# Performance work log

Hardware: AMD Instinct MI355X
Metric: run time of the kernel (lower is better)

Reference implementation:

```python
import jax, jax.numpy as jnp
import numpy as np

EPS = 1e-5
TCOUNT = 18  # SBNet tiles per spatial dim -> 10x10 px tiles on 180x180 map
NUM_HEADS = 6
NUM_ATTRS = 5


def _conv(x, w, groups=1):
    # 3x3 stride-1 'SAME' conv, NCHW / OIHW
    return jax.lax.conv_general_dilated(
        x, w, window_strides=(1, 1), padding='SAME',
        dimension_numbers=('NCHW', 'OIHW', 'NCHW'),
        feature_group_count=groups)


def _bn(y, g, b, m, v):
    scale = g / jnp.sqrt(v + EPS)
    return y * scale[None, :, None, None] + (b - m * scale)[None, :, None, None]


def _mask_px(tile_mask, H, W):
    # expand [B, ty, tx] tile activity to per-pixel mask [B, 1, H, W]
    ty, tx = tile_mask.shape[1], tile_mask.shape[2]
    m = tile_mask.astype(jnp.float32)
    m = jnp.repeat(jnp.repeat(m, H // ty, axis=1), W // tx, axis=2)
    return m[:, None]


def setup_inputs() -> dict:
    key = jax.random.key(0)
    ks = jax.random.split(key, 24)
    B, C, H, W = 2, 512, 180, 180
    SC = 64                       # SHARED_CONV_CHANNEL
    HM1 = SC * NUM_HEADS          # 384
    HM2 = 2 * NUM_HEADS           # hm_max_ch * num_heads = 12
    AT1 = SC * NUM_HEADS * NUM_ATTRS  # 1920
    AT2 = 3 * NUM_ATTRS * NUM_HEADS   # attr_max_ch * 5 * 6 = 90

    def w(k, o, i):
        return jax.random.normal(k, (o, i, 3, 3), jnp.float32) * (1.0 / np.sqrt(i * 9))

    inp = {
        'x': jax.random.normal(ks[0], (B, C, H, W), jnp.float32),
        'tile_mask': jax.random.randint(ks[1], (B, TCOUNT, TCOUNT), 0, 2, jnp.int32),
        'w_shared': w(ks[2], SC, C),
        'g_s': jax.random.uniform(ks[3], (SC,), jnp.float32, 0.5, 1.5),
        'b_s': jax.random.normal(ks[4], (SC,)) * 0.1,
        'm_s': jax.random.normal(ks[5], (SC,)) * 0.1,
        'v_s': jax.random.uniform(ks[6], (SC,), jnp.float32, 0.5, 1.5),
        'w_hm1': w(ks[7], HM1, SC),
        'g_h': jax.random.uniform(ks[8], (HM1,), jnp.float32, 0.5, 1.5),
        'b_h': jax.random.normal(ks[9], (HM1,)) * 0.1,
        'm_h': jax.random.normal(ks[10], (HM1,)) * 0.1,
        'v_h': jax.random.uniform(ks[11], (HM1,), jnp.float32, 0.5, 1.5),
        'w_hm2': w(ks[12], HM2, SC),  # groups=6 -> in_per_group = 384/6 = 64
        'bias_hm': jnp.full((HM2,), -2.19, jnp.float32),  # fill_bias(-2.19)
        'w_attr1': w(ks[13], AT1, SC),
        'g_a': jax.random.uniform(ks[14], (AT1,), jnp.float32, 0.5, 1.5),
        'b_a': jax.random.normal(ks[15], (AT1,)) * 0.1,
        'm_a': jax.random.normal(ks[16], (AT1,)) * 0.1,
        'v_a': jax.random.uniform(ks[17], (AT1,), jnp.float32, 0.5, 1.5),
        'w_attr2': w(ks[18], AT2, SC),  # groups=30 -> in_per_group = 1920/30 = 64
        'bias_attr': jnp.zeros((AT2,), jnp.float32),
    }
    return inp


def reference(x, tile_mask, w_shared, g_s, b_s, m_s, v_s,
              w_hm1, g_h, b_h, m_h, v_h, w_hm2, bias_hm,
              w_attr1, g_a, b_a, m_a, v_a, w_attr2, bias_attr):
    B, _, H, W = x.shape
    mp = _mask_px(tile_mask, H, W)  # SBNet active-tile scatter mask

    # shared conv: gather active tiles -> conv -> BN -> ReLU -> scatter
    xg = x * mp
    shared = jax.nn.relu(_bn(_conv(xg, w_shared), g_s, b_s, m_s, v_s)) * mp

    # heatmap branch: Conv-BN-ReLU (64 -> 384, groups=1) then grouped conv (groups=6)
    h = jax.nn.relu(_bn(_conv(shared, w_hm1), g_h, b_h, m_h, v_h)) * mp
    hm = (_conv(h, w_hm2, groups=NUM_HEADS) + bias_hm[None, :, None, None]) * mp

    # attribute branch: Conv-BN-ReLU (64 -> 1920, groups=1) then grouped conv (groups=30)
    a = jax.nn.relu(_bn(_conv(shared, w_attr1), g_a, b_a, m_a, v_a)) * mp
    attr = (_conv(a, w_attr2, groups=NUM_HEADS * NUM_ATTRS)
            + bias_attr[None, :, None, None]) * mp

    # per-head slices are static index ranges of these tensors (heatmap_outp_inds /
    # attr_outp_inds); return the full stacked maps concatenated on channels.
    return jnp.concatenate([hm, attr], axis=1)  # [B, 12+90, H, W]
```

## Files before the change

kernel.cpp:

```cpp
#include <hip/hip_runtime.h>
#include <cstdint>

#define TC 18
#define HW 180
#define EPSF 1e-5f

typedef _Float16 half8 __attribute__((ext_vector_type(8)));
typedef _Float16 half4 __attribute__((ext_vector_type(4)));
typedef float f32x4 __attribute__((ext_vector_type(4)));

#define OFF_SHB  0
#define N_SHB    (2*HW*HW*64)
#define OFF_WSH  (N_SHB)
#define N_WSH    (9*64*512)
#define OFF_WM   (OFF_WSH + N_WSH)
#define N_WM     (36*9*64*64)
#define OFF_W2   (OFF_WM + N_WM)
#define N_W2     (36*9*16*64)

__global__ __launch_bounds__(256) void prep_kernel(
    const float* __restrict__ w_s, const float* __restrict__ w_hm1,
    const float* __restrict__ w_attr1, const float* __restrict__ w_hm2,
    const float* __restrict__ w_attr2, _Float16* __restrict__ ws) {
  int i = blockIdx.x * 256 + threadIdx.x;
  if (i < N_WSH) {
    int ic = i & 511, oc = (i >> 9) & 63, tap = i >> 15;
    ws[OFF_WSH + i] = (_Float16)w_s[((size_t)(oc*512 + ic))*9 + tap];
    return;
  }
  i -= N_WSH;
  if (i < N_WM) {
    int ic = i & 63, oc = (i >> 6) & 63, tap = (i >> 12) % 9, g = i / 36864;
    float v;
    if (g < 6) v = w_hm1[((size_t)((g*64 + oc)*64 + ic))*9 + tap];
    else       v = w_attr1[((size_t)(((g-6)*64 + oc)*64 + ic))*9 + tap];
    ws[OFF_WM + i] = (_Float16)v;
    return;
  }
  i -= N_WM;
  if (i < N_W2) {
    int ic = i & 63, oc = (i >> 6) & 15, tap = (i >> 10) % 9, g = i / 9216;
    float v = 0.f;
    if (g < 6) { if (oc < 2) v = w_hm2[((size_t)((g*2 + oc)*64 + ic))*9 + tap]; }
    else       { if (oc < 3) v = w_attr2[((size_t)(((g-6)*3 + oc)*64 + ic))*9 + tap]; }
    ws[OFF_W2 + i] = (_Float16)v;
  }
}

__global__ __launch_bounds__(256, 4) void shared_conv_mfma(
    const float* __restrict__ x, const int* __restrict__ tmask,
    const _Float16* __restrict__ wsh,
    const float* __restrict__ g_s, const float* __restrict__ b_s,
    const float* __restrict__ m_s, const float* __restrict__ v_s,
    _Float16* __restrict__ shb) {
  int bid = blockIdx.x;
  int b = bid / (TC*TC), t = bid % (TC*TC);
  int ty = t / TC, tx = t % TC;
  int Y0 = ty*10, X0 = tx*10;
  int tid = threadIdx.x;
  _Float16* shp = shb + (size_t)b*HW*HW*64;
  bool active = tmask[b*TC*TC + t] != 0;
  if (!active) {
    for (int i = tid; i < 1600; i += 256) {
      int px = i >> 4, q = i & 15;
      int gy = Y0 + px/10, gx = X0 + px%10;
      *(float2*)(shp + ((size_t)(gy*HW + gx))*64 + q*4) = make_float2(0.f, 0.f);
    }
    return;
  }
  int nact = 0;
  #pragma unroll
  for (int dy = 0; dy < 3; dy++)
    #pragma unroll
    for (int dx = 0; dx < 3; dx++) {
      int tyy = ty+dy-1, txx = tx+dx-1;
      int a = (tyy>=0 && tyy<TC && txx>=0 && txx<TC) ? tmask[b*TC*TC + tyy*TC + txx] : 0;
      nact |= (a != 0) << (dy*3+dx);
    }
  __shared__ _Float16 sm[144*64];
  int lane = tid & 63, w = tid >> 6;
  int mh = w >> 1, nh = w & 1;
  int l15 = lane & 15, l4 = lane >> 4;
  int r0[4];
  #pragma unroll
  for (int fi = 0; fi < 4; fi++) {
    int f = mh + fi*2;
    int p = f*16 + l15; if (p > 99) p = 99;
    r0[fi] = (p/10)*12 + (p%10);
  }
  f32x4 acc[4][2];
  #pragma unroll
  for (int fi = 0; fi < 4; fi++)
    #pragma unroll
    for (int j = 0; j < 2; j++) acc[fi][j] = (f32x4)0.f;

  for (int ck = 0; ck < 8; ck++) {
    __syncthreads();
    for (int i = tid; i < 1152; i += 256) {
      int px = i % 144, s8 = i / 144;
      int ry = px/12, rx = px%12;
      int gy = Y0-1+ry, gx = X0-1+rx;
      int selr = (ry==0)?0:((ry<=10)?1:2);
      int selc = (rx==0)?0:((rx<=10)?1:2);
      bool ok = (gy>=0 && gy<HW && gx>=0 && gx<HW) && ((nact>>(selr*3+selc))&1);
      half8 hv;
      #pragma unroll
      for (int j = 0; j < 8; j++) hv[j] = (_Float16)0.f;
      if (ok) {
        const float* xp = x + (((size_t)b*512 + ck*64 + s8*8)*HW + gy)*HW + gx;
        #pragma unroll
        for (int j = 0; j < 8; j++) hv[j] = (_Float16)xp[(size_t)j*HW*HW];
      }
      *(half8*)((char*)sm + px*128 + (((s8 ^ (px&7)) & 7)<<4)) = hv;
    }
    __syncthreads();
    for (int tap = 0; tap < 9; tap++) {
      int ky = tap/3, kx = tap%3;
      int radd = ky*12 + kx;
      #pragma unroll
      for (int ks = 0; ks < 2; ks++) {
        half8 bf[2];
        #pragma unroll
        for (int j = 0; j < 2; j++) {
          int oc = (nh*2 + j)*16 + l15;
          bf[j] = *(const half8*)(wsh + (size_t)(tap*64 + oc)*512 + ck*64 + ks*32 + l4*8);
        }
        #pragma unroll
        for (int fi = 0; fi < 4; fi++) {
          int f = mh + fi*2;
          if (f < 7) {
            int r = r0[fi] + radd;
            half8 af = *(const half8*)((const char*)sm + (r<<7) + ((((ks*4 + l4) ^ r) & 7)<<4));
            acc[fi][0] = __builtin_amdgcn_mfma_f32_16x16x32_f16(bf[0], af, acc[fi][0], 0, 0, 0);
            acc[fi][1] = __builtin_amdgcn_mfma_f32_16x16x32_f16(bf[1], af, acc[fi][1], 0, 0, 0);
          }
        }
      }
    }
  }
  float sc4[2][4], sh4[2][4];
  #pragma unroll
  for (int j = 0; j < 2; j++) {
    int ocb = (nh*2 + j)*16 + l4*4;
    float4 gg = *(const float4*)&g_s[ocb];
    float4 vv = *(const float4*)&v_s[ocb];
    float4 bb = *(const float4*)&b_s[ocb];
    float4 mm = *(const float4*)&m_s[ocb];
    float gA[4] = {gg.x,gg.y,gg.z,gg.w}, vA[4] = {vv.x,vv.y,vv.z,vv.w};
    float bA[4] = {bb.x,bb.y,bb.z,bb.w}, mA[4] = {mm.x,mm.y,mm.z,mm.w};
    #pragma unroll
    for (int r = 0; r < 4; r++) {
      float s = gA[r] * rsqrtf(vA[r] + EPSF);
      sc4[j][r] = s; sh4[j][r] = bA[r] - mA[r]*s;
    }
  }
  #pragma unroll
  for (int fi = 0; fi < 4; fi++) {
    int f = mh + fi*2;
    if (f < 7) {
      int p = f*16 + l15;
      if (p < 100) {
        int gy = Y0 + p/10, gx = X0 + p%10;
        _Float16* dst = shp + ((size_t)(gy*HW + gx))*64;
        #pragma unroll
        for (int j = 0; j < 2; j++) {
          int ocb = (nh*2 + j)*16 + l4*4;
          half4 hv;
          #pragma unroll
          for (int r = 0; r < 4; r++)
            hv[r] = (_Float16)fmaxf(fmaf(acc[fi][j][r], sc4[j][r], sh4[j][r]), 0.f);
          *(half4*)(dst + ocb) = hv;
        }
      }
    }
  }
}

__global__ __launch_bounds__(256, 3) void branch_conv_mfma(
    const _Float16* __restrict__ shb, const int* __restrict__ tmask,
    const _Float16* __restrict__ wm, const _Float16* __restrict__ w2,
    const float* __restrict__ g_h, const float* __restrict__ b_h,
    const float* __restrict__ m_h, const float* __restrict__ v_h,
    const float* __restrict__ g_a, const float* __restrict__ b_a,
    const float* __restrict__ m_a, const float* __restrict__ v_a,
    const float* __restrict__ bias_hm, const float* __restrict__ bias_attr,
    float* __restrict__ out) {
  int bid = blockIdx.x;
  int g = bid % 36;
  int t = bid / 36;
  int b = t / (TC*TC); t %= (TC*TC);
  int ty = t / TC, tx = t % TC;
  int Y0 = ty*10, X0 = tx*10;
  int tid = threadIdx.x;
  int Oc = (g < 6) ? 2 : 3;
  int cobase = (g < 6) ? g*2 : 12 + (g-6)*3;
  bool active = tmask[b*TC*TC + ty*TC + tx] != 0;
  if (!active) {
    if (tid < 100) {
      int py = tid/10, px = tid%10;
      for (int o = 0; o < Oc; o++)
        out[(((size_t)b*102 + cobase + o)*HW + (Y0+py))*HW + (X0+px)] = 0.f;
    }
    return;
  }
  int nact = 0;
  #pragma unroll
  for (int dy = 0; dy < 3; dy++)
    #pragma unroll
    for (int dx = 0; dx < 3; dx++) {
      int tyy = ty+dy-1, txx = tx+dx-1;
      int a = (tyy>=0 && tyy<TC && txx>=0 && txx<TC) ? tmask[b*TC*TC + tyy*TC + txx] : 0;
      nact |= (a != 0) << (dy*3+dx);
    }
  __shared__ _Float16 sm[196*64];
  const _Float16* shp = shb + (size_t)b*HW*HW*64;
  int lane = tid & 63, w = tid >> 6;
  int mh = w >> 1, nh = w & 1;
  int l15 = lane & 15, l4 = lane >> 4;

  for (int i = tid; i < 1568; i += 256) {
    int px = i >> 3, s8 = i & 7;
    int ry = px/14, rx = px%14;
    int gy = Y0-2+ry, gx = X0-2+rx;
    half8 hv;
    if (gy>=0 && gy<HW && gx>=0 && gx<HW)
      hv = *(const half8*)(shp + ((size_t)(gy*HW + gx))*64 + s8*8);
    else {
      #pragma unroll
      for (int j = 0; j < 8; j++) hv[j] = (_Float16)0.f;
    }
    *(half8*)((char*)sm + px*128 + (((s8 ^ px) & 7)<<4)) = hv;
  }
  __syncthreads();

  int r0[5];
  #pragma unroll
  for (int fi = 0; fi < 5; fi++) {
    int f = mh + fi*2;
    int p = f*16 + l15; if (p > 143) p = 143;
    r0[fi] = (p/12)*14 + (p%12);
  }
  f32x4 acc[5][2];
  #pragma unroll
  for (int fi = 0; fi < 5; fi++)
    #pragma unroll
    for (int j = 0; j < 2; j++) acc[fi][j] = (f32x4)0.f;

  const _Float16* wmg = wm + (size_t)g*9*64*64;
  for (int tap = 0; tap < 9; tap++) {
    int radd = (tap/3)*14 + (tap%3);
    #pragma unroll
    for (int ks = 0; ks < 2; ks++) {
      half8 bf[2];
      #pragma unroll
      for (int j = 0; j < 2; j++) {
        int oc = (nh*2 + j)*16 + l15;
        bf[j] = *(const half8*)(wmg + (size_t)(tap*64 + oc)*64 + ks*32 + l4*8);
      }
      #pragma unroll
      for (int fi = 0; fi < 5; fi++) {
        int f = mh + fi*2;
        if (f < 9) {
          int r = r0[fi] + radd;
          half8 af = *(const half8*)((const char*)sm + (r<<7) + ((((ks*4 + l4) ^ r) & 7)<<4));
          acc[fi][0] = __builtin_amdgcn_mfma_f32_16x16x32_f16(bf[0], af, acc[fi][0], 0, 0, 0);
          acc[fi][1] = __builtin_amdgcn_mfma_f32_16x16x32_f16(bf[1], af, acc[fi][1], 0, 0, 0);
        }
      }
    }
  }
  __syncthreads();

  {
    float sc4[2][4], sh4[2][4];
    #pragma unroll
    for (int j = 0; j < 2; j++) {
      int ocb = (nh*2 + j)*16 + l4*4;
      int c = ((g < 6) ? g*64 : (g-6)*64) + ocb;
      const float* Gp = (g < 6) ? g_h : g_a;
      const float* Vp = (g < 6) ? v_h : v_a;
      const float* Bp = (g < 6) ? b_h : b_a;
      const float* Mp = (g < 6) ? m_h : m_a;
      float4 gg = *(const float4*)&Gp[c];
      float4 vv = *(const float4*)&Vp[c];
      float4 bb = *(const float4*)&Bp[c];
      float4 mm = *(const float4*)&Mp[c];
      float gA[4] = {gg.x,gg.y,gg.z,gg.w}, vA[4] = {vv.x,vv.y,vv.z,vv.w};
      float bA[4] = {bb.x,bb.y,bb.z,bb.w}, mA[4] = {mm.x,mm.y,mm.z,mm.w};
      #pragma unroll
      for (int r = 0; r < 4; r++) {
        float s = gA[r] * rsqrtf(vA[r] + EPSF);
        sc4[j][r] = s; sh4[j][r] = bA[r] - mA[r]*s;
      }
    }
    #pragma unroll
    for (int fi = 0; fi < 5; fi++) {
      int f = mh + fi*2;
      if (f < 9) {
        int px = f*16 + l15;
        int hy = px/12, hx = px - hy*12;
        int selr = (hy==0)?0:((hy<=10)?1:2);
        int selc = (hx==0)?0:((hx<=10)?1:2);
        bool ok = (nact>>(selr*3+selc)) & 1;
        #pragma unroll
        for (int j = 0; j < 2; j++) {
          int ocb = (nh*2 + j)*16 + l4*4;
          half4 hv;
          #pragma unroll
          for (int r = 0; r < 4; r++) {
            float v = ok ? fmaxf(fmaf(acc[fi][j][r], sc4[j][r], sh4[j][r]), 0.f) : 0.f;
            hv[r] = (_Float16)v;
          }
          *(half4*)((char*)sm + (px<<7) + ((((ocb>>3) ^ px) & 7)<<4) + (ocb&7)*2) = hv;
        }
      }
    }
  }
  __syncthreads();

  int r0b[2];
  #pragma unroll
  for (int fi = 0; fi < 2; fi++) {
    int f = w + fi*4;
    int p = f*16 + l15; if (p > 99) p = 99;
    r0b[fi] = (p/10)*12 + (p%10);
  }
  f32x4 acc2[2];
  acc2[0] = (f32x4)0.f; acc2[1] = (f32x4)0.f;
  const _Float16* w2g = w2 + (size_t)g*9*16*64;
  for (int tap = 0; tap < 9; tap++) {
    int radd = (tap/3)*12 + (tap%3);
    #pragma unroll
    for (int ks = 0; ks < 2; ks++) {
      half8 bf = *(const half8*)(w2g + (size_t)(tap*16 + l15)*64 + ks*32 + l4*8);
      #pragma unroll
      for (int fi = 0; fi < 2; fi++) {
        int f = w + fi*4;
        if (f < 7) {
          int r = r0b[fi] + radd;
          half8 af = *(const half8*)((const char*)sm + (r<<7) + ((((ks*4 + l4) ^ r) & 7)<<4));
          acc2[fi] = __builtin_amdgcn_mfma_f32_16x16x32_f16(bf, af, acc2[fi], 0, 0, 0);
        }
      }
    }
  }
  float bo[3];
  #pragma unroll
  for (int o = 0; o < 3; o++)
    bo[o] = (o < Oc) ? ((g < 6) ? bias_hm[g*2 + o] : bias_attr[(g-6)*3 + o]) : 0.f;
  #pragma unroll
  for (int fi = 0; fi < 2; fi++) {
    int f = w + fi*4;
    int p = f*16 + l15;
    if (f < 7 && l4 == 0 && p < 100) {
      int gy = Y0 + p/10, gx = X0 + p%10;
      float* op = out + (((size_t)b*102 + cobase)*HW + gy)*HW + gx;
      #pragma unroll
      for (int o = 0; o < 3; o++)
        if (o < Oc) op[(size_t)o*HW*HW] = acc2[fi][o] + bo[o];
    }
  }
}

extern "C" void kernel_launch(void* const* d_in, const int* in_sizes, int n_in,
                              void* d_out, int out_size, void* d_ws, size_t ws_size,
                              hipStream_t stream) {
  const float* x        = (const float*)d_in[0];
  const int*   tmask    = (const int*)  d_in[1];
  const float* w_s      = (const float*)d_in[2];
  const float* g_s      = (const float*)d_in[3];
  const float* b_s      = (const float*)d_in[4];
  const float* m_s      = (const float*)d_in[5];
  const float* v_s      = (const float*)d_in[6];
  const float* w_hm1    = (const float*)d_in[7];
  const float* g_h      = (const float*)d_in[8];
  const float* b_h      = (const float*)d_in[9];
  const float* m_h      = (const float*)d_in[10];
  const float* v_h      = (const float*)d_in[11];
  const float* w_hm2    = (const float*)d_in[12];
  const float* bias_hm  = (const float*)d_in[13];
  const float* w_attr1  = (const float*)d_in[14];
  const float* g_a      = (const float*)d_in[15];
  const float* b_a      = (const float*)d_in[16];
  const float* m_a      = (const float*)d_in[17];
  const float* v_a      = (const float*)d_in[18];
  const float* w_attr2  = (const float*)d_in[19];
  const float* bias_attr= (const float*)d_in[20];
  _Float16* ws = (_Float16*)d_ws;
  float* out = (float*)d_out;

  int prep_total = N_WSH + N_WM + N_W2;
  prep_kernel<<<(prep_total + 255)/256, 256, 0, stream>>>(
      w_s, w_hm1, w_attr1, w_hm2, w_attr2, ws);
  shared_conv_mfma<<<2*TC*TC, 256, 0, stream>>>(
      x, tmask, ws + OFF_WSH, g_s, b_s, m_s, v_s, ws + OFF_SHB);
  branch_conv_mfma<<<2*TC*TC*36, 256, 0, stream>>>(
      ws + OFF_SHB, tmask, ws + OFF_WM, ws + OFF_W2,
      g_h, b_h, m_h, v_h, g_a, b_a, m_a, v_a, bias_hm, bias_attr, out);
}
```

Baseline: 658.6 us.

## Process two channel groups per block sharing one staged input halo tile

Each block of the branch conv now handles two of the 36 channel groups instead of one, so the shared-conv halo tile is loaded into LDS once for both groups and the grid is halved. Each wave pair computes all 64 output channels for one group, and the intermediate activations are written to two LDS buffers in two synchronized phases so that the second group does not overwrite the input still being read by the first. This removes half of the global-to-LDS staging traffic and the per-block setup cost. In exchange it uses more LDS and doubles the accumulator registers per wave (20 instead of 10 MFMA tiles), which may reduce occupancy under launch_bounds(256,3).

```diff
diff --git a/kernel.cpp b/kernel.cpp
--- a/kernel.cpp
+++ b/kernel.cpp
@@ -186,20 +186,24 @@
     const float* __restrict__ bias_hm, const float* __restrict__ bias_attr,
     float* __restrict__ out) {
   int bid = blockIdx.x;
-  int g = bid % 36;
-  int t = bid / 36;
+  int g2 = bid % 18;
+  int t = bid / 18;
   int b = t / (TC*TC); t %= (TC*TC);
   int ty = t / TC, tx = t % TC;
   int Y0 = ty*10, X0 = tx*10;
   int tid = threadIdx.x;
-  int Oc = (g < 6) ? 2 : 3;
-  int cobase = (g < 6) ? g*2 : 12 + (g-6)*3;
   bool active = tmask[b*TC*TC + ty*TC + tx] != 0;
   if (!active) {
     if (tid < 100) {
-      int py = tid/10, px = tid%10;
-      for (int o = 0; o < Oc; o++)
-        out[(((size_t)b*102 + cobase + o)*HW + (Y0+py))*HW + (X0+px)] = 0.f;
+      int py = tid/10, pxx = tid%10;
+      #pragma unroll
+      for (int gi = 0; gi < 2; gi++) {
+        int g = g2*2 + gi;
+        int Oc = (g < 6) ? 2 : 3;
+        int cobase = (g < 6) ? g*2 : 12 + (g-6)*3;
+        for (int o = 0; o < Oc; o++)
+          out[(((size_t)b*102 + cobase + o)*HW + (Y0+py))*HW + (X0+pxx)] = 0.f;
+      }
     }
     return;
   }
@@ -212,10 +216,11 @@
       int a = (tyy>=0 && tyy<TC && txx>=0 && txx<TC) ? tmask[b*TC*TC + tyy*TC + txx] : 0;
       nact |= (a != 0) << (dy*3+dx);
     }
-  __shared__ _Float16 sm[196*64];
+  __shared__ _Float16 sm[(196 + 144)*64];
   const _Float16* shp = shb + (size_t)b*HW*HW*64;
   int lane = tid & 63, w = tid >> 6;
-  int mh = w >> 1, nh = w & 1;
+  int gi = w & 1, m = w >> 1;
+  int g = g2*2 + gi;
   int l15 = lane & 15, l4 = lane >> 4;
 
   for (int i = tid; i < 1568; i += 256) {
@@ -236,97 +241,103 @@
   int r0[5];
   #pragma unroll
   for (int fi = 0; fi < 5; fi++) {
-    int f = mh + fi*2;
-    int p = f*16 + l15; if (p > 143) p = 143;
+    int gf = m*5 + fi;
+    int p = gf*16 + l15; if (p > 143) p = 143;
     r0[fi] = (p/12)*14 + (p%12);
   }
-  f32x4 acc[5][2];
+  f32x4 acc[5][4];
   #pragma unroll
   for (int fi = 0; fi < 5; fi++)
     #pragma unroll
-    for (int j = 0; j < 2; j++) acc[fi][j] = (f32x4)0.f;
+    for (int nf = 0; nf < 4; nf++) acc[fi][nf] = (f32x4)0.f;
 
   const _Float16* wmg = wm + (size_t)g*9*64*64;
   for (int tap = 0; tap < 9; tap++) {
     int radd = (tap/3)*14 + (tap%3);
     #pragma unroll
     for (int ks = 0; ks < 2; ks++) {
-      half8 bf[2];
-      #pragma unroll
-      for (int j = 0; j < 2; j++) {
-        int oc = (nh*2 + j)*16 + l15;
-        bf[j] = *(const half8*)(wmg + (size_t)(tap*64 + oc)*64 + ks*32 + l4*8);
-      }
+      half8 bf[4];
+      #pragma unroll
+      for (int nf = 0; nf < 4; nf++)
+        bf[nf] = *(const half8*)(wmg + (size_t)(tap*64 + nf*16 + l15)*64 + ks*32 + l4*8);
       #pragma unroll
       for (int fi = 0; fi < 5; fi++) {
-        int f = mh + fi*2;
-        if (f < 9) {
+        int gf = m*5 + fi;
+        if (gf < 9) {
           int r = r0[fi] + radd;
           half8 af = *(const half8*)((const char*)sm + (r<<7) + ((((ks*4 + l4) ^ r) & 7)<<4));
-          acc[fi][0] = __builtin_amdgcn_mfma_f32_16x16x32_f16(bf[0], af, acc[fi][0], 0, 0, 0);
-          acc[fi][1] = __builtin_amdgcn_mfma_f32_16x16x32_f16(bf[1], af, acc[fi][1], 0, 0, 0);
-        }
-      }
-    }
-  }
-  __syncthreads();
+          #pragma unroll
+          for (int nf = 0; nf < 4; nf++)
+            acc[fi][nf] = __builtin_amdgcn_mfma_f32_16x16x32_f16(bf[nf], af, acc[fi][nf], 0, 0, 0);
+        }
+      }
+    }
+  }
 
   {
-    float sc4[2][4], sh4[2][4];
-    #pragma unroll
-    for (int j = 0; j < 2; j++) {
-      int ocb = (nh*2 + j)*16 + l4*4;
-      int c = ((g < 6) ? g*64 : (g-6)*64) + ocb;
-      const float* Gp = (g < 6) ? g_h : g_a;
-      const float* Vp = (g < 6) ? v_h : v_a;
-      const float* Bp = (g < 6) ? b_h : b_a;
-      const float* Mp = (g < 6) ? m_h : m_a;
-      float4 gg = *(const float4*)&Gp[c];
-      float4 vv = *(const float4*)&Vp[c];
-      float4 bb = *(const float4*)&Bp[c];
-      float4 mm = *(const float4*)&Mp[c];
+    int cbase = (g < 6) ? g*64 : (g-6)*64;
+    const float* GG = (g < 6) ? g_h : g_a;
+    const float* VV = (g < 6) ? v_h : v_a;
+    const float* BB = (g < 6) ? b_h : b_a;
+    const float* MM = (g < 6) ? m_h : m_a;
+    float sc4[4][4], sh4[4][4];
+    #pragma unroll
+    for (int nf = 0; nf < 4; nf++) {
+      int c = cbase + nf*16 + l4*4;
+      float4 gg = *(const float4*)&GG[c];
+      float4 vv = *(const float4*)&VV[c];
+      float4 bb = *(const float4*)&BB[c];
+      float4 mm = *(const float4*)&MM[c];
       float gA[4] = {gg.x,gg.y,gg.z,gg.w}, vA[4] = {vv.x,vv.y,vv.z,vv.w};
       float bA[4] = {bb.x,bb.y,bb.z,bb.w}, mA[4] = {mm.x,mm.y,mm.z,mm.w};
       #pragma unroll
       for (int r = 0; r < 4; r++) {
         float s = gA[r] * rsqrtf(vA[r] + EPSF);
-        sc4[j][r] = s; sh4[j][r] = bA[r] - mA[r]*s;
-      }
-    }
-    #pragma unroll
-    for (int fi = 0; fi < 5; fi++) {
-      int f = mh + fi*2;
-      if (f < 9) {
-        int px = f*16 + l15;
-        int hy = px/12, hx = px - hy*12;
-        int selr = (hy==0)?0:((hy<=10)?1:2);
-        int selc = (hx==0)?0:((hx<=10)?1:2);
-        bool ok = (nact>>(selr*3+selc)) & 1;
+        sc4[nf][r] = s; sh4[nf][r] = bA[r] - mA[r]*s;
+      }
+    }
+    #pragma unroll
+    for (int phase = 0; phase < 2; phase++) {
+      if (gi == phase) {
+        _Float16* hb = (phase == 0) ? (_Float16*)sm + 196*64 : (_Float16*)sm;
         #pragma unroll
-        for (int j = 0; j < 2; j++) {
-          int ocb = (nh*2 + j)*16 + l4*4;
-          half4 hv;
-          #pragma unroll
-          for (int r = 0; r < 4; r++) {
-            float v = ok ? fmaxf(fmaf(acc[fi][j][r], sc4[j][r], sh4[j][r]), 0.f) : 0.f;
-            hv[r] = (_Float16)v;
+        for (int fi = 0; fi < 5; fi++) {
+          int gf = m*5 + fi;
+          if (gf < 9) {
+            int px = gf*16 + l15;
+            int hy = px/12, hx = px - hy*12;
+            int selr = (hy==0)?0:((hy<=10)?1:2);
+            int selc = (hx==0)?0:((hx<=10)?1:2);
+            bool ok = (nact>>(selr*3+selc)) & 1;
+            #pragma unroll
+            for (int nf = 0; nf < 4; nf++) {
+              int ocb = nf*16 + l4*4;
+              half4 hv;
+              #pragma unroll
+              for (int r = 0; r < 4; r++) {
+                float v = ok ? fmaxf(fmaf(acc[fi][nf][r], sc4[nf][r], sh4[nf][r]), 0.f) : 0.f;
+                hv[r] = (_Float16)v;
+              }
+              *(half4*)((char*)hb + (px<<7) + ((((ocb>>3) ^ px) & 7)<<4) + (ocb&7)*2) = hv;
+            }
           }
-          *(half4*)((char*)sm + (px<<7) + ((((ocb>>3) ^ px) & 7)<<4) + (ocb&7)*2) = hv;
-        }
-      }
-    }
-  }
-  __syncthreads();
-
-  int r0b[2];
-  #pragma unroll
-  for (int fi = 0; fi < 2; fi++) {
-    int f = w + fi*4;
+        }
+      }
+      __syncthreads();
+    }
+  }
+
+  const _Float16* hb = (gi == 0) ? (const _Float16*)sm + 196*64 : (const _Float16*)sm;
+  int r0b[4];
+  #pragma unroll
+  for (int fi = 0; fi < 4; fi++) {
+    int f = m*4 + fi;
     int p = f*16 + l15; if (p > 99) p = 99;
     r0b[fi] = (p/10)*12 + (p%10);
   }
-  f32x4 acc2[2];
-  acc2[0] = (f32x4)0.f; acc2[1] = (f32x4)0.f;
+  f32x4 acc2[4];
+  #pragma unroll
+  for (int fi = 0; fi < 4; fi++) acc2[fi] = (f32x4)0.f;
   const _Float16* w2g = w2 + (size_t)g*9*16*64;
   for (int tap = 0; tap < 9; tap++) {
     int radd = (tap/3)*12 + (tap%3);
@@ -334,23 +345,25 @@
     for (int ks = 0; ks < 2; ks++) {
       half8 bf = *(const half8*)(w2g + (size_t)(tap*16 + l15)*64 + ks*32 + l4*8);
       #pragma unroll
-      for (int fi = 0; fi < 2; fi++) {
-        int f = w + fi*4;
+      for (int fi = 0; fi < 4; fi++) {
+        int f = m*4 + fi;
         if (f < 7) {
           int r = r0b[fi] + radd;
-          half8 af = *(const half8*)((const char*)sm + (r<<7) + ((((ks*4 + l4) ^ r) & 7)<<4));
+          half8 af = *(const half8*)((const char*)hb + (r<<7) + ((((ks*4 + l4) ^ r) & 7)<<4));
           acc2[fi] = __builtin_amdgcn_mfma_f32_16x16x32_f16(bf, af, acc2[fi], 0, 0, 0);
         }
       }
     }
   }
+  int Oc = (g < 6) ? 2 : 3;
+  int cobase = (g < 6) ? g*2 : 12 + (g-6)*3;
   float bo[3];
   #pragma unroll
   for (int o = 0; o < 3; o++)
     bo[o] = (o < Oc) ? ((g < 6) ? bias_hm[g*2 + o] : bias_attr[(g-6)*3 + o]) : 0.f;
   #pragma unroll
-  for (int fi = 0; fi < 2; fi++) {
-    int f = w + fi*4;
+  for (int fi = 0; fi < 4; fi++) {
+    int f = m*4 + fi;
     int p = f*16 + l15;
     if (f < 7 && l4 == 0 && p < 100) {
       int gy = Y0 + p/10, gx = X0 + p%10;
@@ -394,7 +407,7 @@
       w_s, w_hm1, w_attr1, w_hm2, w_attr2, ws);
   shared_conv_mfma<<<2*TC*TC, 256, 0, stream>>>(
       x, tmask, ws + OFF_WSH, g_s, b_s, m_s, v_s, ws + OFF_SHB);
-  branch_conv_mfma<<<2*TC*TC*36, 256, 0, stream>>>(
+  branch_conv_mfma<<<2*TC*TC*18, 256, 0, stream>>>(
       ws + OFF_SHB, tmask, ws + OFF_WM, ws + OFF_W2,
       g_h, b_h, m_h, v_h, g_a, b_a, m_a, v_a, bias_hm, bias_attr, out);
 }
```

New measurement: 655.4 us. No clear change (-0.5%).
